# Kernel tuning notes

Hardware: AMD Instinct MI355X
Metric: run time of the kernel (lower is better)

The kernel has to match this reference:

```python
import jax, jax.numpy as jnp
import numpy as np

B, T, C = 2, 2048, 1024
H = 16
HS = C // H
EPS = 1e-5


def layernorm(x, g, b):
    mu = jnp.mean(x, axis=-1, keepdims=True)
    var = jnp.var(x, axis=-1, keepdims=True)
    return (x - mu) * jax.lax.rsqrt(var + EPS) * g + b


def setup_inputs() -> dict:
    key = jax.random.key(0)
    ks = jax.random.split(key, 12)
    s_in = 1.0 / np.sqrt(C)
    s_ff = 1.0 / np.sqrt(4 * C)
    return {
        "x": jax.random.normal(ks[0], (B, T, C), jnp.float32),
        "Wq": jax.random.normal(ks[1], (H, C, HS), jnp.float32) * s_in,
        "Wk": jax.random.normal(ks[2], (H, C, HS), jnp.float32) * s_in,
        "Wv": jax.random.normal(ks[3], (H, C, HS), jnp.float32) * s_in,
        "Wo": jax.random.normal(ks[4], (C, C), jnp.float32) * s_in,
        "bo": jnp.zeros((C,), jnp.float32),
        "W1": jax.random.normal(ks[5], (C, 4 * C), jnp.float32) * s_in,
        "b1": jnp.zeros((4 * C,), jnp.float32),
        "W2": jax.random.normal(ks[6], (4 * C, C), jnp.float32) * s_ff,
        "b2": jnp.zeros((C,), jnp.float32),
        "g1": jnp.ones((C,), jnp.float32),
        "be1": jnp.zeros((C,), jnp.float32),
        "g2": jnp.ones((C,), jnp.float32),
        "be2": jnp.zeros((C,), jnp.float32),
    }


def reference(x, Wq, Wk, Wv, Wo, bo, W1, b1, W2, b2, g1, be1, g2, be2):
    # x: [B,T,C]. Dropout is identity (eval mode).
    x = layernorm(x, g1, be1)
    # --- multi-head causal self-attention (per-source: scale by C**-0.5, NOT head_size) ---
    q = jnp.einsum("btc,hcd->bhtd", x, Wq)
    k = jnp.einsum("btc,hcd->bhtd", x, Wk)
    v = jnp.einsum("btc,hcd->bhtd", x, Wv)
    scores = jnp.einsum("bhtd,bhsd->bhts", q, k) * (C ** -0.5)  # [B,H,T,T]
    causal = jnp.tril(jnp.ones((T, T), bool))
    scores = jnp.where(causal, scores, -jnp.inf)
    wei = jax.nn.softmax(scores, axis=-1)
    attn = jnp.einsum("bhts,bhsd->bhtd", wei, v)
    attn = attn.transpose(0, 2, 1, 3).reshape(B, T, C)  # concat heads on last dim
    sa = attn @ Wo + bo
    x = x + sa
    # --- MLP with second pre-op LayerNorm ---
    x = layernorm(x, g2, be2)
    h = jax.nn.relu(x @ W1 + b1)
    x = x + (h @ W2 + b2)
    return x
```

## Files before the change

kernel.cpp:

```cpp
#include <hip/hip_runtime.h>
#include <hip/hip_bf16.h>
#include <math.h>

#define B_ 2
#define T_ 2048
#define C_ 1024
#define H_ 16
#define HS_ 64
#define N_ROWS (B_*T_)
#define MB (1024*1024)

typedef __attribute__((ext_vector_type(8))) short bf16x8;
typedef __attribute__((ext_vector_type(8))) unsigned short u16x8;
typedef __attribute__((ext_vector_type(4))) float floatx4;

static __device__ __forceinline__ unsigned short f2bf(float f) {
  union { float f; unsigned u; } v; v.f = f;
  unsigned r = v.u + 0x7fff + ((v.u >> 16) & 1);
  return (unsigned short)(r >> 16);
}
static __device__ __forceinline__ float bf2f(unsigned short s) {
  union { unsigned u; float f; } v; v.u = ((unsigned)s) << 16;
  return v.f;
}

__global__ __launch_bounds__(256) void ln_kernel(
    const float* __restrict__ x, const float* __restrict__ g,
    const float* __restrict__ b, unsigned short* __restrict__ outb)
{
  const int row = blockIdx.x;
  const int tid = threadIdx.x;
  const float* xr = x + (size_t)row * C_;
  float4 xv = *reinterpret_cast<const float4*>(xr + tid * 4);
  float s  = xv.x + xv.y + xv.z + xv.w;
  float ss = xv.x*xv.x + xv.y*xv.y + xv.z*xv.z + xv.w*xv.w;
  #pragma unroll
  for (int off = 32; off > 0; off >>= 1) {
    s  += __shfl_down(s, off, 64);
    ss += __shfl_down(ss, off, 64);
  }
  __shared__ float rs[4], rss[4];
  __shared__ float smu, srstd;
  if ((tid & 63) == 0) { rs[tid >> 6] = s; rss[tid >> 6] = ss; }
  __syncthreads();
  if (tid == 0) {
    float S  = rs[0] + rs[1] + rs[2] + rs[3];
    float SS = rss[0] + rss[1] + rss[2] + rss[3];
    float mu  = S * (1.0f / C_);
    float var = SS * (1.0f / C_) - mu * mu;
    smu = mu; srstd = rsqrtf(var + 1e-5f);
  }
  __syncthreads();
  const float mu = smu, rstd = srstd;
  float4 gv = *reinterpret_cast<const float4*>(g + tid * 4);
  float4 bv = *reinterpret_cast<const float4*>(b + tid * 4);
  union { unsigned long long ll; unsigned short s[4]; } o;
  o.s[0] = f2bf((xv.x - mu) * rstd * gv.x + bv.x);
  o.s[1] = f2bf((xv.y - mu) * rstd * gv.y + bv.y);
  o.s[2] = f2bf((xv.z - mu) * rstd * gv.z + bv.z);
  o.s[3] = f2bf((xv.w - mu) * rstd * gv.w + bv.w);
  *reinterpret_cast<unsigned long long*>(outb + (size_t)row * C_ + tid * 4) = o.ll;
}

__global__ __launch_bounds__(256) void transpose_cast(
    const float* __restrict__ in, unsigned short* __restrict__ out, int R, int Cc)
{
  __shared__ float tile[32][33];
  const int bz = blockIdx.z;
  in  += (size_t)bz * R * Cc;
  out += (size_t)bz * R * Cc;
  const int tx = threadIdx.x & 31;
  const int ty = threadIdx.x >> 5;
  const int c0 = blockIdx.x * 32, r0 = blockIdx.y * 32;
  #pragma unroll
  for (int j = 0; j < 4; ++j)
    tile[ty + j*8][tx] = in[(size_t)(r0 + ty + j*8) * Cc + c0 + tx];
  __syncthreads();
  #pragma unroll
  for (int j = 0; j < 4; ++j)
    out[(size_t)(c0 + ty + j*8) * R + r0 + tx] = f2bf(tile[tx][ty + j*8]);
}

template<int TNB, bool OUTBF16, bool RELU, bool HASB, bool HASRES>
__global__ __launch_bounds__(256) void gemm_bf16(
    const unsigned short* __restrict__ A,
    const unsigned short* __restrict__ Bt,
    const float* __restrict__ bias,
    const unsigned short* __restrict__ res,
    void* __restrict__ Cout,
    int M, int N, int K)
{
  constexpr int NT = TNB / 32;
  constexpr int WN = TNB / 2;
  __shared__ unsigned short As[128 * 32];
  __shared__ unsigned short Bs[TNB * 32];
  const int tid  = threadIdx.x;
  const int lane = tid & 63;
  const int wave = tid >> 6;
  const int wm = wave & 1, wn = wave >> 1;
  const int m0 = blockIdx.x * 128, n0 = blockIdx.y * TNB;

  const int lrow = lane >> 2;
  const int lcol = (lane & 3) * 8;
  const int fr = lane & 15;
  const int fq = lane >> 4;

  floatx4 acc[4][NT] = {};

  const unsigned short* Aw = A  + (size_t)m0 * K;
  const unsigned short* Bw = Bt + (size_t)n0 * K;

  for (int k0 = 0; k0 < K; k0 += 32) {
    __syncthreads();
    #pragma unroll
    for (int i = 0; i < 2; ++i) {
      const int rbase = i * 64 + wave * 16;
      const unsigned short* gp = Aw + (size_t)(rbase + lrow) * K + k0 + lcol;
      __builtin_amdgcn_global_load_lds(
          (const __attribute__((address_space(1))) void*)gp,
          (__attribute__((address_space(3))) void*)(As + rbase * 32),
          16, 0, 0);
    }
    #pragma unroll
    for (int i = 0; i < TNB / 64; ++i) {
      const int rbase = i * 64 + wave * 16;
      const unsigned short* gp = Bw + (size_t)(rbase + lrow) * K + k0 + lcol;
      __builtin_amdgcn_global_load_lds(
          (const __attribute__((address_space(1))) void*)gp,
          (__attribute__((address_space(3))) void*)(Bs + rbase * 32),
          16, 0, 0);
    }
    __syncthreads();

    bf16x8 af[4], bfr[NT];
    #pragma unroll
    for (int t = 0; t < 4; ++t)
      af[t]  = *reinterpret_cast<const bf16x8*>(As + (wm*64 + t*16 + fr)*32 + fq*8);
    #pragma unroll
    for (int t = 0; t < NT; ++t)
      bfr[t] = *reinterpret_cast<const bf16x8*>(Bs + (wn*WN + t*16 + fr)*32 + fq*8);
    #pragma unroll
    for (int mt = 0; mt < 4; ++mt)
      #pragma unroll
      for (int nt = 0; nt < NT; ++nt)
        acc[mt][nt] = __builtin_amdgcn_mfma_f32_16x16x32_bf16(
            af[mt], bfr[nt], acc[mt][nt], 0, 0, 0);
  }

  #pragma unroll
  for (int nt = 0; nt < NT; ++nt) {
    const int col = n0 + wn*WN + nt*16 + fr;
    const float bv = HASB ? bias[col] : 0.0f;
    #pragma unroll
    for (int mt = 0; mt < 4; ++mt) {
      #pragma unroll
      for (int r = 0; r < 4; ++r) {
        const int row = m0 + wm*64 + mt*16 + fq*4 + r;
        float v = acc[mt][nt][r] + bv;
        if (RELU) v = v > 0.0f ? v : 0.0f;
        if (HASRES) v += bf2f(res[(size_t)row * N + col]);
        if (OUTBF16) ((unsigned short*)Cout)[(size_t)row * N + col] = f2bf(v);
        else         ((float*)Cout)[(size_t)row * N + col] = v;
      }
    }
  }
}

__global__ __launch_bounds__(256) void v_transpose(
    const unsigned short* __restrict__ qkv, unsigned short* __restrict__ vt)
{
  __shared__ __align__(16) unsigned short sT[64][72];
  const int st = blockIdx.x;
  const int bh = blockIdx.y;
  const int b = bh >> 4, h = bh & 15;
  const int t = threadIdx.x;
  const int r = t >> 2, c0 = (t & 3) * 16;
  const unsigned short* src =
      qkv + (size_t)(b * T_ + st * 64 + r) * 3072 + 2048 + h * 64 + c0;
  *(u16x8*)&sT[r][c0]     = *(const u16x8*)src;
  *(u16x8*)&sT[r][c0 + 8] = *(const u16x8*)(src + 8);
  __syncthreads();
  const int d = t >> 2, sc = (t & 3) * 16;
  unsigned short v[16];
  #pragma unroll
  for (int j = 0; j < 16; ++j) v[j] = sT[sc + j][d];
  unsigned short* dst = vt + ((size_t)bh * 64 + d) * (size_t)T_ + st * 64 + sc;
  *(uint4*)dst       = *(uint4*)&v[0];
  *(uint4*)(dst + 8) = *(uint4*)&v[8];
}

__global__ __launch_bounds__(256, 4) void attn_mfma(
    const unsigned short* __restrict__ qkv,
    const unsigned short* __restrict__ vt,
    unsigned short* __restrict__ out)
{
  const int bh = blockIdx.x;
  const int qt = (int)(gridDim.y - 1) - (int)blockIdx.y;
  const int b = bh >> 4, h = bh & 15;
  const int tid = threadIdx.x;
  const int w = tid >> 6;
  const int lane = tid & 63;
  const int l15 = lane & 15, fq = lane >> 4;
  const int t0 = qt * 64;
  const int q_row = t0 + w * 16 + l15;

  __shared__ __align__(16) unsigned short sK [64][72];
  __shared__ __align__(16) unsigned short sVt[64][72];
  __shared__ __align__(16) unsigned short sP [64][72];

  bf16x8 aq[2];
  {
    const unsigned short* qp = qkv + (size_t)(b*T_ + q_row)*3072 + h*HS_ + fq*8;
    aq[0] = *(const bf16x8*)qp;
    aq[1] = *(const bf16x8*)(qp + 32);
  }

  floatx4 oacc[4] = {};
  float m_s = -3.0e38f, l_s = 0.0f;
  const float c1 = 1.4426950408889634f / 32.0f;
  const int nks = qt + 1;

  for (int ks = 0; ks < nks; ++ks) {
    __syncthreads();
    {
      const int r = tid >> 2, c0 = (tid & 3) * 16;
      const unsigned short* kp =
          qkv + (size_t)(b*T_ + ks*64 + r)*3072 + C_ + h*HS_ + c0;
      u16x8 k0 = *(const u16x8*)kp, k1 = *(const u16x8*)(kp + 8);
      const unsigned short* vp =
          vt + ((size_t)bh*64 + r)*(size_t)T_ + ks*64 + c0;
      u16x8 v0 = *(const u16x8*)vp, v1 = *(const u16x8*)(vp + 8);
      *(u16x8*)&sK[r][c0]      = k0; *(u16x8*)&sK[r][c0 + 8]  = k1;
      *(u16x8*)&sVt[r][c0]     = v0; *(u16x8*)&sVt[r][c0 + 8] = v1;
    }
    __syncthreads();

    floatx4 stacc[4] = {};
    #pragma unroll
    for (int st = 0; st < 4; ++st) {
      bf16x8 k0 = *(const bf16x8*)&sK[st*16 + l15][fq*8];
      bf16x8 k1 = *(const bf16x8*)&sK[st*16 + l15][32 + fq*8];
      stacc[st] = __builtin_amdgcn_mfma_f32_16x16x32_bf16(k0, aq[0], stacc[st], 0, 0, 0);
      stacc[st] = __builtin_amdgcn_mfma_f32_16x16x32_bf16(k1, aq[1], stacc[st], 0, 0, 0);
    }

    if (ks == qt) {
      #pragma unroll
      for (int st = 0; st < 4; ++st)
        #pragma unroll
        for (int r = 0; r < 4; ++r) {
          const int s = ks*64 + st*16 + fq*4 + r;
          if (s > q_row) stacc[st][r] = -3.0e38f;
        }
    }

    float mx = -3.0e38f;
    #pragma unroll
    for (int st = 0; st < 4; ++st)
      #pragma unroll
      for (int r = 0; r < 4; ++r) mx = fmaxf(mx, stacc[st][r]);
    mx = fmaxf(mx, __shfl_xor(mx, 16, 64));
    mx = fmaxf(mx, __shfl_xor(mx, 32, 64));
    const float mnew = fmaxf(m_s, mx);
    const float alpha = exp2f((m_s - mnew) * c1);
    m_s = mnew;

    float sum = 0.0f;
    #pragma unroll
    for (int st = 0; st < 4; ++st) {
      unsigned pu[4];
      #pragma unroll
      for (int r = 0; r < 4; ++r) {
        const float p = exp2f((stacc[st][r] - mnew) * c1);
        sum += p;
        union { float f; unsigned u; } cv; cv.f = p;
        pu[r] = cv.u + 0x8000u;
      }
      const unsigned lo = __builtin_amdgcn_perm(pu[1], pu[0], 0x07060302u);
      const unsigned hi = __builtin_amdgcn_perm(pu[3], pu[2], 0x07060302u);
      const unsigned long long pk = ((unsigned long long)hi << 32) | lo;
      *(unsigned long long*)&sP[w*16 + l15][st*16 + fq*4] = pk;
    }
    sum += __shfl_xor(sum, 16, 64);
    sum += __shfl_xor(sum, 32, 64);
    l_s = l_s * alpha + sum;

    #pragma unroll
    for (int r = 0; r < 4; ++r) {
      const float ar = __shfl(alpha, fq*4 + r, 64);
      #pragma unroll
      for (int dt = 0; dt < 4; ++dt) oacc[dt][r] *= ar;
    }

    #pragma unroll
    for (int c = 0; c < 2; ++c) {
      bf16x8 ap = *(const bf16x8*)&sP[w*16 + l15][c*32 + fq*8];
      #pragma unroll
      for (int dt = 0; dt < 4; ++dt) {
        bf16x8 bv = *(const bf16x8*)&sVt[dt*16 + l15][c*32 + fq*8];
        oacc[dt] = __builtin_amdgcn_mfma_f32_16x16x32_bf16(ap, bv, oacc[dt], 0, 0, 0);
      }
    }
  }

  #pragma unroll
  for (int r = 0; r < 4; ++r) {
    const float il = 1.0f / __shfl(l_s, fq*4 + r, 64);
    const int q = t0 + w*16 + fq*4 + r;
    #pragma unroll
    for (int dt = 0; dt < 4; ++dt)
      out[(size_t)(b*T_ + q)*C_ + h*HS_ + dt*16 + l15] = f2bf(oacc[dt][r] * il);
  }
}

extern "C" void kernel_launch(void* const* d_in, const int* in_sizes, int n_in,
                              void* d_out, int out_size, void* d_ws, size_t ws_size,
                              hipStream_t stream)
{
  const float* x   = (const float*)d_in[0];
  const float* Wq  = (const float*)d_in[1];
  const float* Wk  = (const float*)d_in[2];
  const float* Wv  = (const float*)d_in[3];
  const float* Wo  = (const float*)d_in[4];
  const float* bo  = (const float*)d_in[5];
  const float* W1  = (const float*)d_in[6];
  const float* b1  = (const float*)d_in[7];
  const float* W2  = (const float*)d_in[8];
  const float* b2  = (const float*)d_in[9];
  const float* g1  = (const float*)d_in[10];
  const float* be1 = (const float*)d_in[11];
  const float* g2  = (const float*)d_in[12];
  const float* be2 = (const float*)d_in[13];
  float* out = (float*)d_out;

  char* ws = (char*)d_ws;
  unsigned short* BtQKV = (unsigned short*)(ws + (size_t) 0*MB);
  unsigned short* BtWo  = (unsigned short*)(ws + (size_t) 6*MB);
  unsigned short* BtW1  = (unsigned short*)(ws + (size_t) 8*MB);
  unsigned short* BtW2  = (unsigned short*)(ws + (size_t)16*MB);
  unsigned short* lnb   = (unsigned short*)(ws + (size_t)24*MB);
  unsigned short* qkvb  = (unsigned short*)(ws + (size_t)32*MB);
  unsigned short* vtb   = (unsigned short*)(ws + (size_t)56*MB);
  unsigned short* attnb = (unsigned short*)(ws + (size_t)64*MB);
  float*          x2    = (float*)         (ws + (size_t)32*MB);
  unsigned short* hb    = (unsigned short*)(ws + (size_t)32*MB);

  dim3 blk(256);

  transpose_cast<<<dim3(HS_/32, C_/32, H_), blk, 0, stream>>>(Wq, BtQKV,               C_, HS_);
  transpose_cast<<<dim3(HS_/32, C_/32, H_), blk, 0, stream>>>(Wk, BtQKV + 1024*1024,   C_, HS_);
  transpose_cast<<<dim3(HS_/32, C_/32, H_), blk, 0, stream>>>(Wv, BtQKV + 2*1024*1024, C_, HS_);
  transpose_cast<<<dim3(C_/32,  C_/32, 1),  blk, 0, stream>>>(Wo, BtWo, C_, C_);
  transpose_cast<<<dim3(4*C_/32,C_/32, 1),  blk, 0, stream>>>(W1, BtW1, C_, 4*C_);
  transpose_cast<<<dim3(C_/32,4*C_/32, 1),  blk, 0, stream>>>(W2, BtW2, 4*C_, C_);

  ln_kernel<<<dim3(N_ROWS), blk, 0, stream>>>(x, g1, be1, lnb);

  gemm_bf16<128,true,false,false,false><<<dim3(N_ROWS/128, 3072/128), blk, 0, stream>>>(
      lnb, BtQKV, nullptr, nullptr, qkvb, N_ROWS, 3072, C_);

  v_transpose<<<dim3(T_/64, B_*H_), blk, 0, stream>>>(qkvb, vtb);

  attn_mfma<<<dim3(B_*H_, T_/64), blk, 0, stream>>>(qkvb, vtb, attnb);

  gemm_bf16<64,false,false,true,true><<<dim3(N_ROWS/128, C_/64), blk, 0, stream>>>(
      attnb, BtWo, bo, lnb, x2, N_ROWS, C_, C_);

  ln_kernel<<<dim3(N_ROWS), blk, 0, stream>>>(x2, g2, be2, lnb);

  gemm_bf16<128,true,true,true,false><<<dim3(N_ROWS/128, 4*C_/128), blk, 0, stream>>>(
      lnb, BtW1, b1, nullptr, hb, N_ROWS, 4*C_, C_);

  gemm_bf16<64,false,false,true,true><<<dim3(N_ROWS/128, C_/64), blk, 0, stream>>>(
      hb, BtW2, b2, lnb, out, N_ROWS, C_, 4*C_);
}
```

Before: 391.5 us.

## Split the W2 GEMM along K into two halves with a separate reduce kernel

The final FFN down-projection GEMM (K=4096) is split along K into two launches' worth of blocks via gridDim.z=2. Each half writes fp32 partial sums to workspace buffers, and a new elementwise kernel adds the two partials, the bias and the residual. The aim is to double the block count for a GEMM that otherwise launches only 512 blocks, improving CU occupancy. In exchange it adds roughly 32 MB of extra fp32 partial traffic, one more kernel launch, and reuses workspace regions that previously held weights and activations.

```diff
diff --git a/kernel.cpp b/kernel.cpp
--- a/kernel.cpp
+++ b/kernel.cpp
@@ -164,6 +164,105 @@
       }
     }
   }
+}
+
+template<int TNB>
+__global__ __launch_bounds__(256) void gemm_splitk(
+    const unsigned short* __restrict__ A,
+    const unsigned short* __restrict__ Bt,
+    float* __restrict__ C0,
+    float* __restrict__ C1,
+    int M, int N, int Kfull)
+{
+  constexpr int NT = TNB / 32;
+  constexpr int WN = TNB / 2;
+  __shared__ unsigned short As[128 * 32];
+  __shared__ unsigned short Bs[TNB * 32];
+  const int tid  = threadIdx.x;
+  const int lane = tid & 63;
+  const int wave = tid >> 6;
+  const int wm = wave & 1, wn = wave >> 1;
+  const int m0 = blockIdx.x * 128, n0 = blockIdx.y * TNB;
+  const int z  = blockIdx.z;
+  const int Kh = Kfull >> 1;
+
+  const int lrow = lane >> 2;
+  const int lcol = (lane & 3) * 8;
+  const int fr = lane & 15;
+  const int fq = lane >> 4;
+
+  floatx4 acc[4][NT] = {};
+
+  const unsigned short* Aw = A  + (size_t)m0 * Kfull + (size_t)z * Kh;
+  const unsigned short* Bw = Bt + (size_t)n0 * Kfull + (size_t)z * Kh;
+  float* Cw = z ? C1 : C0;
+
+  for (int k0 = 0; k0 < Kh; k0 += 32) {
+    __syncthreads();
+    #pragma unroll
+    for (int i = 0; i < 2; ++i) {
+      const int rbase = i * 64 + wave * 16;
+      const unsigned short* gp = Aw + (size_t)(rbase + lrow) * Kfull + k0 + lcol;
+      __builtin_amdgcn_global_load_lds(
+          (const __attribute__((address_space(1))) void*)gp,
+          (__attribute__((address_space(3))) void*)(As + rbase * 32),
+          16, 0, 0);
+    }
+    #pragma unroll
+    for (int i = 0; i < TNB / 64; ++i) {
+      const int rbase = i * 64 + wave * 16;
+      const unsigned short* gp = Bw + (size_t)(rbase + lrow) * Kfull + k0 + lcol;
+      __builtin_amdgcn_global_load_lds(
+          (const __attribute__((address_space(1))) void*)gp,
+          (__attribute__((address_space(3))) void*)(Bs + rbase * 32),
+          16, 0, 0);
+    }
+    __syncthreads();
+
+    bf16x8 af[4], bfr[NT];
+    #pragma unroll
+    for (int t = 0; t < 4; ++t)
+      af[t]  = *reinterpret_cast<const bf16x8*>(As + (wm*64 + t*16 + fr)*32 + fq*8);
+    #pragma unroll
+    for (int t = 0; t < NT; ++t)
+      bfr[t] = *reinterpret_cast<const bf16x8*>(Bs + (wn*WN + t*16 + fr)*32 + fq*8);
+    #pragma unroll
+    for (int mt = 0; mt < 4; ++mt)
+      #pragma unroll
+      for (int nt = 0; nt < NT; ++nt)
+        acc[mt][nt] = __builtin_amdgcn_mfma_f32_16x16x32_bf16(
+            af[mt], bfr[nt], acc[mt][nt], 0, 0, 0);
+  }
+
+  #pragma unroll
+  for (int nt = 0; nt < NT; ++nt) {
+    const int col = n0 + wn*WN + nt*16 + fr;
+    #pragma unroll
+    for (int mt = 0; mt < 4; ++mt)
+      #pragma unroll
+      for (int r = 0; r < 4; ++r) {
+        const int row = m0 + wm*64 + mt*16 + fq*4 + r;
+        Cw[(size_t)row * N + col] = acc[mt][nt][r];
+      }
+  }
+}
+
+__global__ __launch_bounds__(256) void splitk_reduce(
+    const float* __restrict__ p0, const float* __restrict__ p1,
+    const float* __restrict__ bias, const unsigned short* __restrict__ res,
+    float* __restrict__ out)
+{
+  const size_t i = ((size_t)blockIdx.x * 256 + threadIdx.x) * 4;
+  float4 a = *reinterpret_cast<const float4*>(p0 + i);
+  float4 b = *reinterpret_cast<const float4*>(p1 + i);
+  float4 bv = *reinterpret_cast<const float4*>(bias + (i & (size_t)(C_ - 1)));
+  const unsigned short* rp = res + i;
+  float4 o;
+  o.x = a.x + b.x + bv.x + bf2f(rp[0]);
+  o.y = a.y + b.y + bv.y + bf2f(rp[1]);
+  o.z = a.z + b.z + bv.z + bf2f(rp[2]);
+  o.w = a.w + b.w + bv.w + bf2f(rp[3]);
+  *reinterpret_cast<float4*>(out + i) = o;
 }
 
 __global__ __launch_bounds__(256) void v_transpose(
@@ -344,6 +443,8 @@
   unsigned short* attnb = (unsigned short*)(ws + (size_t)64*MB);
   float*          x2    = (float*)         (ws + (size_t)32*MB);
   unsigned short* hb    = (unsigned short*)(ws + (size_t)32*MB);
+  float*          p0    = (float*)         (ws + (size_t) 0*MB);
+  float*          p1    = (float*)         (ws + (size_t)72*MB);
 
   dim3 blk(256);
 
@@ -371,6 +472,9 @@
   gemm_bf16<128,true,true,true,false><<<dim3(N_ROWS/128, 4*C_/128), blk, 0, stream>>>(
       lnb, BtW1, b1, nullptr, hb, N_ROWS, 4*C_, C_);
 
-  gemm_bf16<64,false,false,true,true><<<dim3(N_ROWS/128, C_/64), blk, 0, stream>>>(
-      hb, BtW2, b2, lnb, out, N_ROWS, C_, 4*C_);
-}
+  gemm_splitk<64><<<dim3(N_ROWS/128, C_/64, 2), blk, 0, stream>>>(
+      hb, BtW2, p0, p1, N_ROWS, C_, 4*C_);
+
+  splitk_reduce<<<dim3((N_ROWS * C_) / (256 * 4)), blk, 0, stream>>>(
+      p0, p1, b2, lnb, out);
+}
```

Result: faster. 382.1 us (-2.4%).
